# Kernel tuning notes

Hardware: AMD Instinct MI355X
Metric: run time of the kernel (lower is better)

The kernel has to match this reference:

```python
import jax, jax.numpy as jnp
import numpy as np

EPS = 1e-5

def conv2x2(x, w, b):
    # x: NCHW, w: OIHW (2x2), stride 2, valid padding
    y = jax.lax.conv_general_dilated(x, w, window_strides=(2, 2), padding='VALID',
                                     dimension_numbers=('NCHW', 'OIHW', 'NCHW'))
    return y + b[None, :, None, None]

def instancenorm(x):
    # per-sample, per-channel norm over H,W; biased variance, no affine (PyTorch defaults)
    mu = jnp.mean(x, axis=(2, 3), keepdims=True)
    var = jnp.mean(jnp.square(x - mu), axis=(2, 3), keepdims=True)
    return (x - mu) * jax.lax.rsqrt(var + EPS)

def lrelu(x):
    return jax.nn.leaky_relu(x, negative_slope=0.01)

def setup_inputs() -> dict:
    key = jax.random.key(0)
    ks = jax.random.split(key, 14)
    B, L = 256, 20
    s = 0.05
    inp = {
        'x': jax.random.normal(ks[0], (B, 3, 128, 128), jnp.float32),
        'labels': jax.random.uniform(ks[1], (B, L), jnp.float32),
        'w1': jax.random.normal(ks[2], (16, 3, 2, 2), jnp.float32) * s,
        'b1': jnp.zeros((16,), jnp.float32),
        'w2': jax.random.normal(ks[3], (32, 16 + L, 2, 2), jnp.float32) * s,
        'b2': jnp.zeros((32,), jnp.float32),
        'w3': jax.random.normal(ks[4], (64, 32, 2, 2), jnp.float32) * s,
        'b3': jnp.zeros((64,), jnp.float32),
        'w4': jax.random.normal(ks[5], (128, 64, 2, 2), jnp.float32) * s,
        'b4': jnp.zeros((128,), jnp.float32),
        'fcw1': jax.random.normal(ks[6], (1024, 128 * 8 * 8), jnp.float32) * s,
        'fcb1': jnp.zeros((1024,), jnp.float32),
        'fcw2': jax.random.normal(ks[7], (1, 1024), jnp.float32) * s,
        'fcb2': jnp.zeros((1,), jnp.float32),
    }
    return inp

def reference(x, labels, w1, b1, w2, b2, w3, b3, w4, b4, fcw1, fcb1, fcw2, fcb2):
    h = lrelu(instancenorm(conv2x2(x, w1, b1)))            # [B,16,64,64]
    # vectorized replacement of the per-element label broadcast loop
    lab = jnp.broadcast_to(labels[:, :, None, None],
                           (h.shape[0], labels.shape[1], h.shape[2], h.shape[3]))
    h = jnp.concatenate([h, lab], axis=1)                  # [B,36,64,64]
    h = lrelu(instancenorm(conv2x2(h, w2, b2)))            # [B,32,32,32]
    h = lrelu(instancenorm(conv2x2(h, w3, b3)))            # [B,64,16,16]
    h = lrelu(instancenorm(conv2x2(h, w4, b4)))            # [B,128,8,8]
    h = h.reshape(h.shape[0], -1)                          # [B,8192]
    h = lrelu(h @ fcw1.T + fcb1)                           # [B,1024]
    return h @ fcw2.T + fcb2                               # [B,1]
```

## Files before the change

kernel.cpp:

```cpp
#include <hip/hip_runtime.h>

#define EPSI 1e-5f

typedef __attribute__((ext_vector_type(8))) short bf16x8;
typedef __attribute__((ext_vector_type(4))) float f32x4;

__device__ __forceinline__ float lrelu(float x) { return x > 0.f ? x : 0.01f * x; }

__device__ __forceinline__ unsigned short f2bf(float x) {
    unsigned int u = __float_as_uint(x);
    return (unsigned short)((u + 0x7fffu + ((u >> 16) & 1u)) >> 16);
}
__device__ __forceinline__ float bflo(unsigned int v) { return __uint_as_float(v << 16); }
__device__ __forceinline__ float bfhi(unsigned int v) { return __uint_as_float(v & 0xFFFF0000u); }
__device__ __forceinline__ unsigned int pack2(float a, float b) {
    return (unsigned int)f2bf(a) | ((unsigned int)f2bf(b) << 16);
}
__device__ __forceinline__ bf16x8 pack8(float4 a, float4 b) {
    union { unsigned short u[8]; bf16x8 v; } p;
    p.u[0] = f2bf(a.x); p.u[1] = f2bf(a.y); p.u[2] = f2bf(a.z); p.u[3] = f2bf(a.w);
    p.u[4] = f2bf(b.x); p.u[5] = f2bf(b.y); p.u[6] = f2bf(b.z); p.u[7] = f2bf(b.w);
    return p.v;
}

__device__ __forceinline__ float2 block_reduce_sum2(float a, float b) {
    #pragma unroll
    for (int off = 1; off < 64; off <<= 1) {
        a += __shfl_xor(a, off, 64);
        b += __shfl_xor(b, off, 64);
    }
    __shared__ float lds[8];
    const int t = threadIdx.x;
    if ((t & 63) == 0) { lds[2 * (t >> 6)] = a; lds[2 * (t >> 6) + 1] = b; }
    __syncthreads();
    a = lds[0] + lds[2] + lds[4] + lds[6];
    b = lds[1] + lds[3] + lds[5] + lds[7];
    return make_float2(a, b);
}


__global__ __launch_bounds__(1024) void wprep(const float* __restrict__ w2,
                                              const float* __restrict__ w3,
                                              const float* __restrict__ w4,
                                              unsigned short* __restrict__ wk) {
    const int g = blockIdx.x * 1024 + threadIdx.x;
    if (g < 2048) {
        const int co = g >> 6, k = g & 63;
        const int ic = (k >> 4) * 4 + (k & 3), row = (k >> 3) & 1, tx = (k >> 2) & 1;
        wk[g] = f2bf(w2[co * 144 + ic * 4 + row * 2 + tx]);
    } else if (g < 10240) {
        const int e = g - 2048, co = e >> 7, k = e & 127;
        const int ic = (k >> 4) * 4 + (k & 3), row = (k >> 3) & 1, tx = (k >> 2) & 1;
        wk[g] = f2bf(w3[co * 128 + ic * 4 + row * 2 + tx]);
    } else if (g < 43008) {
        const int e = g - 10240, co = e >> 8, k = e & 255;
        const int ic = (k >> 4) * 4 + (k & 3), row = (k >> 3) & 1, tx = (k >> 2) & 1;
        wk[g] = f2bf(w4[co * 256 + ic * 4 + row * 2 + tx]);
    }
}

__global__ __launch_bounds__(1024, 1) void k1_conv_in(const float* __restrict__ x,
                                                      const float* __restrict__ w1,
                                                      unsigned short* __restrict__ h1) {
    const int n = blockIdx.x;
    const int t = threadIdx.x;
    __shared__ float red[16][16][2];
    __shared__ float msc[16][2];
    const float* xn = x + (size_t)n * 49152;
    float acc[16][4];
    #pragma unroll
    for (int j = 0; j < 16; ++j)
        #pragma unroll
        for (int q = 0; q < 4; ++q) acc[j][q] = 0.f;
    #pragma unroll 1
    for (int ic = 0; ic < 3; ++ic) {
        const float* p = xn + ic * 16384;
        float2 v0[4], v1[4];
        #pragma unroll
        for (int q = 0; q < 4; ++q) {
            const int idx = t + 1024 * q;
            const int oy = idx >> 6, ox = idx & 63;
            v0[q] = ((const float2*)(p + (2 * oy) * 128))[ox];
            v1[q] = ((const float2*)(p + (2 * oy + 1) * 128))[ox];
        }
        #pragma unroll
        for (int j = 0; j < 16; ++j) {
            const float4 wv = *(const float4*)(w1 + j * 12 + ic * 4);
            #pragma unroll
            for (int q = 0; q < 4; ++q)
                acc[j][q] += v0[q].x * wv.x + v0[q].y * wv.y + v1[q].x * wv.z + v1[q].y * wv.w;
        }
    }
    const int w = t >> 6, l = t & 63;
    #pragma unroll
    for (int j = 0; j < 16; ++j) {
        float s1 = acc[j][0] + acc[j][1] + acc[j][2] + acc[j][3];
        float s2 = acc[j][0] * acc[j][0] + acc[j][1] * acc[j][1] +
                   acc[j][2] * acc[j][2] + acc[j][3] * acc[j][3];
        #pragma unroll
        for (int off = 1; off < 64; off <<= 1) {
            s1 += __shfl_xor(s1, off, 64);
            s2 += __shfl_xor(s2, off, 64);
        }
        if (l == 0) { red[w][j][0] = s1; red[w][j][1] = s2; }
    }
    __syncthreads();
    if (t < 16) {
        float s1 = 0.f, s2 = 0.f;
        #pragma unroll
        for (int ww = 0; ww < 16; ++ww) { s1 += red[ww][t][0]; s2 += red[ww][t][1]; }
        const float mean = s1 * (1.f / 4096.f);
        const float var = s2 * (1.f / 4096.f) - mean * mean;
        msc[t][0] = mean; msc[t][1] = rsqrtf(var + EPSI);
    }
    __syncthreads();
    unsigned short* on = h1 + (size_t)n * 65536;
    #pragma unroll
    for (int q = 0; q < 4; ++q) {
        const int px = t + 1024 * q;
        #pragma unroll
        for (int q4 = 0; q4 < 4; ++q4) {
            const float n0 = lrelu((acc[4 * q4 + 0][q] - msc[4 * q4 + 0][0]) * msc[4 * q4 + 0][1]);
            const float n1 = lrelu((acc[4 * q4 + 1][q] - msc[4 * q4 + 1][0]) * msc[4 * q4 + 1][1]);
            const float n2 = lrelu((acc[4 * q4 + 2][q] - msc[4 * q4 + 2][0]) * msc[4 * q4 + 2][1]);
            const float n3 = lrelu((acc[4 * q4 + 3][q] - msc[4 * q4 + 3][0]) * msc[4 * q4 + 3][1]);
            uint2 u; u.x = pack2(n0, n1); u.y = pack2(n2, n3);
            *(uint2*)(on + ((size_t)q4 * 4096 + px) * 4) = u;
        }
    }
}

__global__ __launch_bounds__(1024, 1) void k2m(const unsigned short* __restrict__ h1,
                                               const unsigned short* __restrict__ wk,
                                               unsigned short* __restrict__ h2) {
    const int n = blockIdx.x;
    const int t = threadIdx.x;
    const int w = t >> 6, l = t & 63;
    __shared__ float red[16][32][2];
    __shared__ float msc[32][2];
    const unsigned short* h1n = h1 + (size_t)n * 65536;
    bf16x8 af[2][2];
    #pragma unroll
    for (int cf = 0; cf < 2; ++cf)
        #pragma unroll
        for (int ks = 0; ks < 2; ++ks)
            af[cf][ks] = *(const bf16x8*)(wk + (cf * 16 + (l & 15)) * 64 + ks * 32 + (l >> 4) * 8);
    f32x4 acc[4][2];
    const f32x4 z = {0.f, 0.f, 0.f, 0.f};
    #pragma unroll
    for (int pg = 0; pg < 4; ++pg) { acc[pg][0] = z; acc[pg][1] = z; }
    const int row = (l >> 4) & 1, icq0 = (l >> 4) >> 1;
    #pragma unroll
    for (int pg = 0; pg < 4; ++pg) {
        const int oy = 2 * w + (pg >> 1);
        const int ox = (pg & 1) * 16 + (l & 15);
        #pragma unroll
        for (int ks = 0; ks < 2; ++ks) {
            const bf16x8 bv = *(const bf16x8*)(h1n + (ks * 2 + icq0) * 16384 + (2 * oy + row) * 256 + ox * 8);
            acc[pg][0] = __builtin_amdgcn_mfma_f32_16x16x32_bf16(af[0][ks], bv, acc[pg][0], 0, 0, 0);
            acc[pg][1] = __builtin_amdgcn_mfma_f32_16x16x32_bf16(af[1][ks], bv, acc[pg][1], 0, 0, 0);
        }
    }
    #pragma unroll
    for (int cf = 0; cf < 2; ++cf) {
        #pragma unroll
        for (int r = 0; r < 4; ++r) {
            float s1 = acc[0][cf][r] + acc[1][cf][r] + acc[2][cf][r] + acc[3][cf][r];
            float s2 = acc[0][cf][r] * acc[0][cf][r] + acc[1][cf][r] * acc[1][cf][r] +
                       acc[2][cf][r] * acc[2][cf][r] + acc[3][cf][r] * acc[3][cf][r];
            #pragma unroll
            for (int off = 1; off < 16; off <<= 1) {
                s1 += __shfl_xor(s1, off, 64);
                s2 += __shfl_xor(s2, off, 64);
            }
            if ((l & 15) == 0) {
                red[w][cf * 16 + (l >> 4) * 4 + r][0] = s1;
                red[w][cf * 16 + (l >> 4) * 4 + r][1] = s2;
            }
        }
    }
    __syncthreads();
    if (t < 32) {
        float s1 = 0.f, s2 = 0.f;
        #pragma unroll
        for (int ww = 0; ww < 16; ++ww) { s1 += red[ww][t][0]; s2 += red[ww][t][1]; }
        const float mean = s1 * (1.f / 1024.f);
        const float var = s2 * (1.f / 1024.f) - mean * mean;
        msc[t][0] = mean; msc[t][1] = rsqrtf(var + EPSI);
    }
    __syncthreads();
    unsigned short* on = h2 + (size_t)n * 32768;
    #pragma unroll
    for (int pg = 0; pg < 4; ++pg) {
        const int px = w * 64 + pg * 16 + (l & 15);
        #pragma unroll
        for (int cf = 0; cf < 2; ++cf) {
            const int co0 = cf * 16 + (l >> 4) * 4;
            float v[4];
            #pragma unroll
            for (int r = 0; r < 4; ++r)
                v[r] = lrelu((acc[pg][cf][r] - msc[co0 + r][0]) * msc[co0 + r][1]);
            uint2 u; u.x = pack2(v[0], v[1]); u.y = pack2(v[2], v[3]);
            *(uint2*)(on + ((size_t)(cf * 4 + (l >> 4)) * 1024 + px) * 4) = u;
        }
    }
}

__global__ __launch_bounds__(1024, 1) void k3m(const unsigned short* __restrict__ h2,
                                               const unsigned short* __restrict__ wk,
                                               unsigned short* __restrict__ h3) {
    const int n = blockIdx.x;
    const int t = threadIdx.x;
    const int w = t >> 6, l = t & 63;
    __shared__ float red[16][64][2];
    __shared__ float msc[64][2];
    const unsigned short* h2n = h2 + (size_t)n * 32768;
    f32x4 acc[4];
    const f32x4 z = {0.f, 0.f, 0.f, 0.f};
    #pragma unroll
    for (int cf = 0; cf < 4; ++cf) acc[cf] = z;
    const int row = (l >> 4) & 1, icq0 = (l >> 4) >> 1;
    #pragma unroll
    for (int ks = 0; ks < 4; ++ks) {
        const bf16x8 bv = *(const bf16x8*)(h2n + (ks * 2 + icq0) * 4096 + (2 * w + row) * 128 + (l & 15) * 8);
        #pragma unroll
        for (int cf = 0; cf < 4; ++cf) {
            const bf16x8 af = *(const bf16x8*)(wk + (cf * 16 + (l & 15)) * 128 + ks * 32 + (l >> 4) * 8);
            acc[cf] = __builtin_amdgcn_mfma_f32_16x16x32_bf16(af, bv, acc[cf], 0, 0, 0);
        }
    }
    #pragma unroll
    for (int cf = 0; cf < 4; ++cf) {
        #pragma unroll
        for (int r = 0; r < 4; ++r) {
            float s1 = acc[cf][r], s2 = acc[cf][r] * acc[cf][r];
            #pragma unroll
            for (int off = 1; off < 16; off <<= 1) {
                s1 += __shfl_xor(s1, off, 64);
                s2 += __shfl_xor(s2, off, 64);
            }
            if ((l & 15) == 0) {
                red[w][cf * 16 + (l >> 4) * 4 + r][0] = s1;
                red[w][cf * 16 + (l >> 4) * 4 + r][1] = s2;
            }
        }
    }
    __syncthreads();
    if (t < 64) {
        float s1 = 0.f, s2 = 0.f;
        #pragma unroll
        for (int ww = 0; ww < 16; ++ww) { s1 += red[ww][t][0]; s2 += red[ww][t][1]; }
        const float mean = s1 * (1.f / 256.f);
        const float var = s2 * (1.f / 256.f) - mean * mean;
        msc[t][0] = mean; msc[t][1] = rsqrtf(var + EPSI);
    }
    __syncthreads();
    unsigned short* on = h3 + (size_t)n * 16384;
    const int px = w * 16 + (l & 15);
    #pragma unroll
    for (int cf = 0; cf < 4; ++cf) {
        const int co0 = cf * 16 + (l >> 4) * 4;
        float v[4];
        #pragma unroll
        for (int r = 0; r < 4; ++r)
            v[r] = lrelu((acc[cf][r] - msc[co0 + r][0]) * msc[co0 + r][1]);
        uint2 u; u.x = pack2(v[0], v[1]); u.y = pack2(v[2], v[3]);
        *(uint2*)(on + ((size_t)(cf * 4 + (l >> 4)) * 256 + px) * 4) = u;
    }
}

__global__ __launch_bounds__(512, 2) void k4m(const unsigned short* __restrict__ h3,
                                              const unsigned short* __restrict__ wk,
                                              unsigned short* __restrict__ h4) {
    const int n = blockIdx.x;
    const int t = threadIdx.x;
    const int w = t >> 6, l = t & 63;
    const int cfp = w & 3, khalf = w >> 2;
    __shared__ float ps[4][64][32];
    const unsigned short* h3n = h3 + (size_t)n * 16384;
    f32x4 acc[4][2];
    const f32x4 z = {0.f, 0.f, 0.f, 0.f};
    #pragma unroll
    for (int pg = 0; pg < 4; ++pg) { acc[pg][0] = z; acc[pg][1] = z; }
    const int row = (l >> 4) & 1, icq0 = (l >> 4) >> 1;
    const int oyb = (l & 15) >> 3, ox = l & 7;
    #pragma unroll
    for (int ksl = 0; ksl < 4; ++ksl) {
        const int ks = khalf * 4 + ksl;
        bf16x8 af0 = *(const bf16x8*)(wk + ((cfp * 2 + 0) * 16 + (l & 15)) * 256 + ks * 32 + (l >> 4) * 8);
        bf16x8 af1 = *(const bf16x8*)(wk + ((cfp * 2 + 1) * 16 + (l & 15)) * 256 + ks * 32 + (l >> 4) * 8);
        #pragma unroll
        for (int pg = 0; pg < 4; ++pg) {
            const int oy = pg * 2 + oyb;
            const bf16x8 bv = *(const bf16x8*)(h3n + (ks * 2 + icq0) * 1024 + (2 * oy + row) * 64 + ox * 8);
            acc[pg][0] = __builtin_amdgcn_mfma_f32_16x16x32_bf16(af0, bv, acc[pg][0], 0, 0, 0);
            acc[pg][1] = __builtin_amdgcn_mfma_f32_16x16x32_bf16(af1, bv, acc[pg][1], 0, 0, 0);
        }
    }
    if (khalf == 0) {
        #pragma unroll
        for (int pg = 0; pg < 4; ++pg)
            #pragma unroll
            for (int cfi = 0; cfi < 2; ++cfi)
                #pragma unroll
                for (int r = 0; r < 4; ++r)
                    ps[cfp][l][pg * 8 + cfi * 4 + r] = acc[pg][cfi][r];
    }
    __syncthreads();
    if (khalf == 1) {
        unsigned short* on = h4 + (size_t)n * 8192;
        #pragma unroll
        for (int cfi = 0; cfi < 2; ++cfi) {
            #pragma unroll
            for (int r = 0; r < 4; ++r) {
                float v[4];
                #pragma unroll
                for (int pg = 0; pg < 4; ++pg)
                    v[pg] = acc[pg][cfi][r] + ps[cfp][l][pg * 8 + cfi * 4 + r];
                float s1 = v[0] + v[1] + v[2] + v[3];
                float s2 = v[0] * v[0] + v[1] * v[1] + v[2] * v[2] + v[3] * v[3];
                #pragma unroll
                for (int off = 1; off < 16; off <<= 1) {
                    s1 += __shfl_xor(s1, off, 64);
                    s2 += __shfl_xor(s2, off, 64);
                }
                const float mean = s1 * (1.f / 64.f);
                const float var = s2 * (1.f / 64.f) - mean * mean;
                const float sc = rsqrtf(var + EPSI);
                const int co = (cfp * 2 + cfi) * 16 + (l >> 4) * 4 + r;
                #pragma unroll
                for (int pg = 0; pg < 4; ++pg)
                    on[co * 64 + pg * 16 + (l & 15)] = f2bf(lrelu((v[pg] - mean) * sc));
            }
        }
    }
}

__global__ __launch_bounds__(256, 2) void k5_fc1(const unsigned short* __restrict__ A,
                                                 const float* __restrict__ Wf,
                                                 float* __restrict__ Cp) {
    __shared__ unsigned short As[128 * 72];
    __shared__ unsigned short Bs[128 * 72];
    const int t = threadIdx.x;
    const int sk = blockIdx.x >> 4;
    const int tile = blockIdx.x & 15;
    const int mt = tile >> 3, nt = tile & 7;
    const int m0 = mt * 128, n0 = nt * 128;
    const int w = t >> 6, l = t & 63;
    const int wm = (w >> 1) * 64, wn = (w & 1) * 64;
    const int lr16 = l & 15, lk8 = (l >> 4) * 8;
    const int srow = t >> 3, scol = (t & 7) * 8;
    f32x4 acc[4][4];
    const f32x4 z = {0.f, 0.f, 0.f, 0.f};
    #pragma unroll
    for (int f = 0; f < 4; ++f)
        #pragma unroll
        for (int g = 0; g < 4; ++g) acc[f][g] = z;
    const int kbeg = sk * 512;
    #pragma unroll 1
    for (int kt = 0; kt < 8; ++kt) {
        const int kc = kbeg + kt * 64;
        bf16x8 av[4], bv[4];
        #pragma unroll
        for (int i = 0; i < 4; ++i) {
            av[i] = *(const bf16x8*)(A + (size_t)(m0 + srow + 32 * i) * 8192 + kc + scol);
            const float4 w0 = *(const float4*)(Wf + (size_t)(n0 + srow + 32 * i) * 8192 + kc + scol);
            const float4 w1 = *(const float4*)(Wf + (size_t)(n0 + srow + 32 * i) * 8192 + kc + scol + 4);
            bv[i] = pack8(w0, w1);
        }
        __syncthreads();
        #pragma unroll
        for (int i = 0; i < 4; ++i) {
            *(bf16x8*)&As[(srow + 32 * i) * 72 + scol] = av[i];
            *(bf16x8*)&Bs[(srow + 32 * i) * 72 + scol] = bv[i];
        }
        __syncthreads();
        #pragma unroll
        for (int ks = 0; ks < 2; ++ks) {
            bf16x8 af[4], bfr[4];
            #pragma unroll
            for (int f = 0; f < 4; ++f)
                af[f] = *(const bf16x8*)&As[(wm + f * 16 + lr16) * 72 + ks * 32 + lk8];
            #pragma unroll
            for (int g = 0; g < 4; ++g)
                bfr[g] = *(const bf16x8*)&Bs[(wn + g * 16 + lr16) * 72 + ks * 32 + lk8];
            #pragma unroll
            for (int f = 0; f < 4; ++f)
                #pragma unroll
                for (int g = 0; g < 4; ++g)
                    acc[f][g] = __builtin_amdgcn_mfma_f32_16x16x32_bf16(af[f], bfr[g], acc[f][g], 0, 0, 0);
        }
    }
    const int orow = (l >> 4) * 4, ocol = l & 15;
    #pragma unroll
    for (int f = 0; f < 4; ++f) {
        #pragma unroll
        for (int g = 0; g < 4; ++g) {
            #pragma unroll
            for (int j = 0; j < 4; ++j) {
                const int m = m0 + wm + f * 16 + orow + j;
                const int nn = n0 + wn + g * 16 + ocol;
                Cp[((size_t)sk * 256 + m) * 1024 + nn] = acc[f][g][j];
            }
        }
    }
}

__global__ __launch_bounds__(256) void k6_fc2(const float* __restrict__ Cp,
                                              const float* __restrict__ bias,
                                              const float* __restrict__ w,
                                              const float* __restrict__ b,
                                              float* __restrict__ out) {
    const int n = blockIdx.x, t = threadIdx.x;
    float part = 0.f;
    #pragma unroll
    for (int i = 0; i < 4; ++i) {
        const int nn = t + 256 * i;
        float s = 0.f;
        #pragma unroll
        for (int sk = 0; sk < 16; ++sk)
            s += Cp[((size_t)sk * 256 + n) * 1024 + nn];
        part += lrelu(s + bias[nn]) * w[nn];
    }
    const float2 red = block_reduce_sum2(part, 0.f);
    if (t == 0) out[n] = red.x + b[0];
}

extern "C" void kernel_launch(void* const* d_in, const int* in_sizes, int n_in,
                              void* d_out, int out_size, void* d_ws, size_t ws_size,
                              hipStream_t stream) {
    (void)in_sizes; (void)n_in; (void)out_size; (void)ws_size;
    const float* x    = (const float*)d_in[0];
    const float* w1   = (const float*)d_in[2];
    const float* w2   = (const float*)d_in[4];
    const float* w3   = (const float*)d_in[6];
    const float* w4   = (const float*)d_in[8];
    const float* fcw1 = (const float*)d_in[10];
    const float* fcb1 = (const float*)d_in[11];
    const float* fcw2 = (const float*)d_in[12];
    const float* fcb2 = (const float*)d_in[13];
    float* out = (float*)d_out;
    float* bufA = (float*)d_ws;
    float* bufB = bufA + 16777216;
    unsigned short* h1 = (unsigned short*)bufA;
    unsigned short* h2 = (unsigned short*)bufB;
    unsigned short* h3 = (unsigned short*)bufA;
    unsigned short* h4 = (unsigned short*)bufB;
    unsigned short* wk = (unsigned short*)bufB + 12582912;
    float* Cp = bufA;
    wprep<<<42, 1024, 0, stream>>>(w2, w3, w4, wk);
    k1_conv_in<<<256, 1024, 0, stream>>>(x, w1, h1);
    k2m<<<256, 1024, 0, stream>>>(h1, wk, h2);
    k3m<<<256, 1024, 0, stream>>>(h2, wk + 2048, h3);
    k4m<<<256, 512, 0, stream>>>(h3, wk + 10240, h4);
    k5_fc1<<<256, 256, 0, stream>>>(h4, fcw1, Cp);
    k6_fc2<<<256, 256, 0, stream>>>(Cp, fcb1, fcw2, fcb2, out);
}
```

Baseline: 92.56 us.

## Fuse conv layers 2-4 into one kernel keeping intermediates in LDS

```diff
diff --git a/kernel.cpp b/kernel.cpp
--- a/kernel.cpp
+++ b/kernel.cpp
@@ -11,8 +11,6 @@
     unsigned int u = __float_as_uint(x);
     return (unsigned short)((u + 0x7fffu + ((u >> 16) & 1u)) >> 16);
 }
-__device__ __forceinline__ float bflo(unsigned int v) { return __uint_as_float(v << 16); }
-__device__ __forceinline__ float bfhi(unsigned int v) { return __uint_as_float(v & 0xFFFF0000u); }
 __device__ __forceinline__ unsigned int pack2(float a, float b) {
     return (unsigned int)f2bf(a) | ((unsigned int)f2bf(b) << 16);
 }
@@ -130,207 +128,203 @@
     }
 }
 
-__global__ __launch_bounds__(1024, 1) void k2m(const unsigned short* __restrict__ h1,
-                                               const unsigned short* __restrict__ wk,
-                                               unsigned short* __restrict__ h2) {
+__global__ __launch_bounds__(1024, 1) void k234(const unsigned short* __restrict__ h1,
+                                                const unsigned short* __restrict__ wk,
+                                                unsigned short* __restrict__ h4) {
     const int n = blockIdx.x;
     const int t = threadIdx.x;
     const int w = t >> 6, l = t & 63;
-    __shared__ float red[16][32][2];
-    __shared__ float msc[32][2];
-    const unsigned short* h1n = h1 + (size_t)n * 65536;
-    bf16x8 af[2][2];
-    #pragma unroll
-    for (int cf = 0; cf < 2; ++cf)
-        #pragma unroll
-        for (int ks = 0; ks < 2; ++ks)
-            af[cf][ks] = *(const bf16x8*)(wk + (cf * 16 + (l & 15)) * 64 + ks * 32 + (l >> 4) * 8);
-    f32x4 acc[4][2];
-    const f32x4 z = {0.f, 0.f, 0.f, 0.f};
-    #pragma unroll
-    for (int pg = 0; pg < 4; ++pg) { acc[pg][0] = z; acc[pg][1] = z; }
-    const int row = (l >> 4) & 1, icq0 = (l >> 4) >> 1;
-    #pragma unroll
-    for (int pg = 0; pg < 4; ++pg) {
-        const int oy = 2 * w + (pg >> 1);
-        const int ox = (pg & 1) * 16 + (l & 15);
-        #pragma unroll
-        for (int ks = 0; ks < 2; ++ks) {
-            const bf16x8 bv = *(const bf16x8*)(h1n + (ks * 2 + icq0) * 16384 + (2 * oy + row) * 256 + ox * 8);
-            acc[pg][0] = __builtin_amdgcn_mfma_f32_16x16x32_bf16(af[0][ks], bv, acc[pg][0], 0, 0, 0);
-            acc[pg][1] = __builtin_amdgcn_mfma_f32_16x16x32_bf16(af[1][ks], bv, acc[pg][1], 0, 0, 0);
-        }
-    }
-    #pragma unroll
-    for (int cf = 0; cf < 2; ++cf) {
-        #pragma unroll
-        for (int r = 0; r < 4; ++r) {
-            float s1 = acc[0][cf][r] + acc[1][cf][r] + acc[2][cf][r] + acc[3][cf][r];
-            float s2 = acc[0][cf][r] * acc[0][cf][r] + acc[1][cf][r] * acc[1][cf][r] +
-                       acc[2][cf][r] * acc[2][cf][r] + acc[3][cf][r] * acc[3][cf][r];
-            #pragma unroll
-            for (int off = 1; off < 16; off <<= 1) {
-                s1 += __shfl_xor(s1, off, 64);
-                s2 += __shfl_xor(s2, off, 64);
-            }
-            if ((l & 15) == 0) {
-                red[w][cf * 16 + (l >> 4) * 4 + r][0] = s1;
-                red[w][cf * 16 + (l >> 4) * 4 + r][1] = s2;
-            }
-        }
-    }
-    __syncthreads();
-    if (t < 32) {
-        float s1 = 0.f, s2 = 0.f;
-        #pragma unroll
-        for (int ww = 0; ww < 16; ++ww) { s1 += red[ww][t][0]; s2 += red[ww][t][1]; }
-        const float mean = s1 * (1.f / 1024.f);
-        const float var = s2 * (1.f / 1024.f) - mean * mean;
-        msc[t][0] = mean; msc[t][1] = rsqrtf(var + EPSI);
-    }
-    __syncthreads();
-    unsigned short* on = h2 + (size_t)n * 32768;
-    #pragma unroll
-    for (int pg = 0; pg < 4; ++pg) {
-        const int px = w * 64 + pg * 16 + (l & 15);
-        #pragma unroll
-        for (int cf = 0; cf < 2; ++cf) {
-            const int co0 = cf * 16 + (l >> 4) * 4;
-            float v[4];
-            #pragma unroll
-            for (int r = 0; r < 4; ++r)
-                v[r] = lrelu((acc[pg][cf][r] - msc[co0 + r][0]) * msc[co0 + r][1]);
-            uint2 u; u.x = pack2(v[0], v[1]); u.y = pack2(v[2], v[3]);
-            *(uint2*)(on + ((size_t)(cf * 4 + (l >> 4)) * 1024 + px) * 4) = u;
-        }
-    }
-}
-
-__global__ __launch_bounds__(1024, 1) void k3m(const unsigned short* __restrict__ h2,
-                                               const unsigned short* __restrict__ wk,
-                                               unsigned short* __restrict__ h3) {
-    const int n = blockIdx.x;
-    const int t = threadIdx.x;
-    const int w = t >> 6, l = t & 63;
+    __shared__ unsigned short h2s[32768];
+    __shared__ unsigned short h3s[16384];
+    __shared__ float ps[4][64][32];
     __shared__ float red[16][64][2];
     __shared__ float msc[64][2];
-    const unsigned short* h2n = h2 + (size_t)n * 32768;
-    f32x4 acc[4];
-    const f32x4 z = {0.f, 0.f, 0.f, 0.f};
-    #pragma unroll
-    for (int cf = 0; cf < 4; ++cf) acc[cf] = z;
-    const int row = (l >> 4) & 1, icq0 = (l >> 4) >> 1;
-    #pragma unroll
-    for (int ks = 0; ks < 4; ++ks) {
-        const bf16x8 bv = *(const bf16x8*)(h2n + (ks * 2 + icq0) * 4096 + (2 * w + row) * 128 + (l & 15) * 8);
-        #pragma unroll
-        for (int cf = 0; cf < 4; ++cf) {
-            const bf16x8 af = *(const bf16x8*)(wk + (cf * 16 + (l & 15)) * 128 + ks * 32 + (l >> 4) * 8);
-            acc[cf] = __builtin_amdgcn_mfma_f32_16x16x32_bf16(af, bv, acc[cf], 0, 0, 0);
-        }
-    }
-    #pragma unroll
-    for (int cf = 0; cf < 4; ++cf) {
-        #pragma unroll
-        for (int r = 0; r < 4; ++r) {
-            float s1 = acc[cf][r], s2 = acc[cf][r] * acc[cf][r];
-            #pragma unroll
-            for (int off = 1; off < 16; off <<= 1) {
-                s1 += __shfl_xor(s1, off, 64);
-                s2 += __shfl_xor(s2, off, 64);
-            }
-            if ((l & 15) == 0) {
-                red[w][cf * 16 + (l >> 4) * 4 + r][0] = s1;
-                red[w][cf * 16 + (l >> 4) * 4 + r][1] = s2;
-            }
-        }
-    }
-    __syncthreads();
-    if (t < 64) {
-        float s1 = 0.f, s2 = 0.f;
-        #pragma unroll
-        for (int ww = 0; ww < 16; ++ww) { s1 += red[ww][t][0]; s2 += red[ww][t][1]; }
-        const float mean = s1 * (1.f / 256.f);
-        const float var = s2 * (1.f / 256.f) - mean * mean;
-        msc[t][0] = mean; msc[t][1] = rsqrtf(var + EPSI);
-    }
-    __syncthreads();
-    unsigned short* on = h3 + (size_t)n * 16384;
-    const int px = w * 16 + (l & 15);
-    #pragma unroll
-    for (int cf = 0; cf < 4; ++cf) {
-        const int co0 = cf * 16 + (l >> 4) * 4;
-        float v[4];
-        #pragma unroll
-        for (int r = 0; r < 4; ++r)
-            v[r] = lrelu((acc[cf][r] - msc[co0 + r][0]) * msc[co0 + r][1]);
-        uint2 u; u.x = pack2(v[0], v[1]); u.y = pack2(v[2], v[3]);
-        *(uint2*)(on + ((size_t)(cf * 4 + (l >> 4)) * 256 + px) * 4) = u;
-    }
-}
-
-__global__ __launch_bounds__(512, 2) void k4m(const unsigned short* __restrict__ h3,
-                                              const unsigned short* __restrict__ wk,
-                                              unsigned short* __restrict__ h4) {
-    const int n = blockIdx.x;
-    const int t = threadIdx.x;
-    const int w = t >> 6, l = t & 63;
-    const int cfp = w & 3, khalf = w >> 2;
-    __shared__ float ps[4][64][32];
-    const unsigned short* h3n = h3 + (size_t)n * 16384;
-    f32x4 acc[4][2];
-    const f32x4 z = {0.f, 0.f, 0.f, 0.f};
-    #pragma unroll
-    for (int pg = 0; pg < 4; ++pg) { acc[pg][0] = z; acc[pg][1] = z; }
-    const int row = (l >> 4) & 1, icq0 = (l >> 4) >> 1;
-    const int oyb = (l & 15) >> 3, ox = l & 7;
-    #pragma unroll
-    for (int ksl = 0; ksl < 4; ++ksl) {
-        const int ks = khalf * 4 + ksl;
-        bf16x8 af0 = *(const bf16x8*)(wk + ((cfp * 2 + 0) * 16 + (l & 15)) * 256 + ks * 32 + (l >> 4) * 8);
-        bf16x8 af1 = *(const bf16x8*)(wk + ((cfp * 2 + 1) * 16 + (l & 15)) * 256 + ks * 32 + (l >> 4) * 8);
+    const unsigned short* h1n = h1 + (size_t)n * 65536;
+
+    {
+        const unsigned short* wk2 = wk;
+        bf16x8 af[2][2];
+        #pragma unroll
+        for (int cf = 0; cf < 2; ++cf)
+            #pragma unroll
+            for (int ks = 0; ks < 2; ++ks)
+                af[cf][ks] = *(const bf16x8*)(wk2 + (cf * 16 + (l & 15)) * 64 + ks * 32 + (l >> 4) * 8);
+        f32x4 acc[4][2];
+        const f32x4 z = {0.f, 0.f, 0.f, 0.f};
+        #pragma unroll
+        for (int pg = 0; pg < 4; ++pg) { acc[pg][0] = z; acc[pg][1] = z; }
+        const int row = (l >> 4) & 1, icq0 = (l >> 4) >> 1;
         #pragma unroll
         for (int pg = 0; pg < 4; ++pg) {
-            const int oy = pg * 2 + oyb;
-            const bf16x8 bv = *(const bf16x8*)(h3n + (ks * 2 + icq0) * 1024 + (2 * oy + row) * 64 + ox * 8);
-            acc[pg][0] = __builtin_amdgcn_mfma_f32_16x16x32_bf16(af0, bv, acc[pg][0], 0, 0, 0);
-            acc[pg][1] = __builtin_amdgcn_mfma_f32_16x16x32_bf16(af1, bv, acc[pg][1], 0, 0, 0);
-        }
-    }
-    if (khalf == 0) {
-        #pragma unroll
-        for (int pg = 0; pg < 4; ++pg)
-            #pragma unroll
-            for (int cfi = 0; cfi < 2; ++cfi)
-                #pragma unroll
-                for (int r = 0; r < 4; ++r)
-                    ps[cfp][l][pg * 8 + cfi * 4 + r] = acc[pg][cfi][r];
-    }
-    __syncthreads();
-    if (khalf == 1) {
-        unsigned short* on = h4 + (size_t)n * 8192;
-        #pragma unroll
-        for (int cfi = 0; cfi < 2; ++cfi) {
+            const int oy = 2 * w + (pg >> 1);
+            const int ox = (pg & 1) * 16 + (l & 15);
+            #pragma unroll
+            for (int ks = 0; ks < 2; ++ks) {
+                const bf16x8 bv = *(const bf16x8*)(h1n + (ks * 2 + icq0) * 16384 + (2 * oy + row) * 256 + ox * 8);
+                acc[pg][0] = __builtin_amdgcn_mfma_f32_16x16x32_bf16(af[0][ks], bv, acc[pg][0], 0, 0, 0);
+                acc[pg][1] = __builtin_amdgcn_mfma_f32_16x16x32_bf16(af[1][ks], bv, acc[pg][1], 0, 0, 0);
+            }
+        }
+        #pragma unroll
+        for (int cf = 0; cf < 2; ++cf) {
             #pragma unroll
             for (int r = 0; r < 4; ++r) {
-                float v[4];
-                #pragma unroll
-                for (int pg = 0; pg < 4; ++pg)
-                    v[pg] = acc[pg][cfi][r] + ps[cfp][l][pg * 8 + cfi * 4 + r];
-                float s1 = v[0] + v[1] + v[2] + v[3];
-                float s2 = v[0] * v[0] + v[1] * v[1] + v[2] * v[2] + v[3] * v[3];
+                float s1 = acc[0][cf][r] + acc[1][cf][r] + acc[2][cf][r] + acc[3][cf][r];
+                float s2 = acc[0][cf][r] * acc[0][cf][r] + acc[1][cf][r] * acc[1][cf][r] +
+                           acc[2][cf][r] * acc[2][cf][r] + acc[3][cf][r] * acc[3][cf][r];
                 #pragma unroll
                 for (int off = 1; off < 16; off <<= 1) {
                     s1 += __shfl_xor(s1, off, 64);
                     s2 += __shfl_xor(s2, off, 64);
                 }
-                const float mean = s1 * (1.f / 64.f);
-                const float var = s2 * (1.f / 64.f) - mean * mean;
-                const float sc = rsqrtf(var + EPSI);
-                const int co = (cfp * 2 + cfi) * 16 + (l >> 4) * 4 + r;
-                #pragma unroll
-                for (int pg = 0; pg < 4; ++pg)
-                    on[co * 64 + pg * 16 + (l & 15)] = f2bf(lrelu((v[pg] - mean) * sc));
+                if ((l & 15) == 0) {
+                    red[w][cf * 16 + (l >> 4) * 4 + r][0] = s1;
+                    red[w][cf * 16 + (l >> 4) * 4 + r][1] = s2;
+                }
+            }
+        }
+        __syncthreads();
+        if (t < 32) {
+            float s1 = 0.f, s2 = 0.f;
+            #pragma unroll
+            for (int ww = 0; ww < 16; ++ww) { s1 += red[ww][t][0]; s2 += red[ww][t][1]; }
+            const float mean = s1 * (1.f / 1024.f);
+            const float var = s2 * (1.f / 1024.f) - mean * mean;
+            msc[t][0] = mean; msc[t][1] = rsqrtf(var + EPSI);
+        }
+        __syncthreads();
+        #pragma unroll
+        for (int pg = 0; pg < 4; ++pg) {
+            const int px = w * 64 + pg * 16 + (l & 15);
+            #pragma unroll
+            for (int cf = 0; cf < 2; ++cf) {
+                const int co0 = cf * 16 + (l >> 4) * 4;
+                float v[4];
+                #pragma unroll
+                for (int r = 0; r < 4; ++r)
+                    v[r] = lrelu((acc[pg][cf][r] - msc[co0 + r][0]) * msc[co0 + r][1]);
+                uint2 u; u.x = pack2(v[0], v[1]); u.y = pack2(v[2], v[3]);
+                *(uint2*)(&h2s[((cf * 4 + (l >> 4)) * 1024 + px) * 4]) = u;
+            }
+        }
+    }
+    __syncthreads();
+
+    {
+        const unsigned short* wk3 = wk + 2048;
+        f32x4 acc[4];
+        const f32x4 z = {0.f, 0.f, 0.f, 0.f};
+        #pragma unroll
+        for (int cf = 0; cf < 4; ++cf) acc[cf] = z;
+        const int row = (l >> 4) & 1, icq0 = (l >> 4) >> 1;
+        #pragma unroll
+        for (int ks = 0; ks < 4; ++ks) {
+            const bf16x8 bv = *(const bf16x8*)(&h2s[(ks * 2 + icq0) * 4096 + (2 * w + row) * 128 + (l & 15) * 8]);
+            #pragma unroll
+            for (int cf = 0; cf < 4; ++cf) {
+                const bf16x8 af = *(const bf16x8*)(wk3 + (cf * 16 + (l & 15)) * 128 + ks * 32 + (l >> 4) * 8);
+                acc[cf] = __builtin_amdgcn_mfma_f32_16x16x32_bf16(af, bv, acc[cf], 0, 0, 0);
+            }
+        }
+        #pragma unroll
+        for (int cf = 0; cf < 4; ++cf) {
+            #pragma unroll
+            for (int r = 0; r < 4; ++r) {
+                float s1 = acc[cf][r], s2 = acc[cf][r] * acc[cf][r];
+                #pragma unroll
+                for (int off = 1; off < 16; off <<= 1) {
+                    s1 += __shfl_xor(s1, off, 64);
+                    s2 += __shfl_xor(s2, off, 64);
+                }
+                if ((l & 15) == 0) {
+                    red[w][cf * 16 + (l >> 4) * 4 + r][0] = s1;
+                    red[w][cf * 16 + (l >> 4) * 4 + r][1] = s2;
+                }
+            }
+        }
+        __syncthreads();
+        if (t < 64) {
+            float s1 = 0.f, s2 = 0.f;
+            #pragma unroll
+            for (int ww = 0; ww < 16; ++ww) { s1 += red[ww][t][0]; s2 += red[ww][t][1]; }
+            const float mean = s1 * (1.f / 256.f);
+            const float var = s2 * (1.f / 256.f) - mean * mean;
+            msc[t][0] = mean; msc[t][1] = rsqrtf(var + EPSI);
+        }
+        __syncthreads();
+        const int px = w * 16 + (l & 15);
+        #pragma unroll
+        for (int cf = 0; cf < 4; ++cf) {
+            const int co0 = cf * 16 + (l >> 4) * 4;
+            float v[4];
+            #pragma unroll
+            for (int r = 0; r < 4; ++r)
+                v[r] = lrelu((acc[cf][r] - msc[co0 + r][0]) * msc[co0 + r][1]);
+            uint2 u; u.x = pack2(v[0], v[1]); u.y = pack2(v[2], v[3]);
+            *(uint2*)(&h3s[((cf * 4 + (l >> 4)) * 256 + px) * 4]) = u;
+        }
+    }
+    __syncthreads();
+
+    {
+        const unsigned short* wk4 = wk + 10240;
+        const int cfp = w & 3, khalf = (w >> 2) & 1;
+        f32x4 acc[4][2];
+        const f32x4 z = {0.f, 0.f, 0.f, 0.f};
+        #pragma unroll
+        for (int pg = 0; pg < 4; ++pg) { acc[pg][0] = z; acc[pg][1] = z; }
+        const int row = (l >> 4) & 1, icq0 = (l >> 4) >> 1;
+        const int oyb = (l & 15) >> 3, ox = l & 7;
+        if (w < 8) {
+            #pragma unroll
+            for (int ksl = 0; ksl < 4; ++ksl) {
+                const int ks = khalf * 4 + ksl;
+                bf16x8 af0 = *(const bf16x8*)(wk4 + ((cfp * 2 + 0) * 16 + (l & 15)) * 256 + ks * 32 + (l >> 4) * 8);
+                bf16x8 af1 = *(const bf16x8*)(wk4 + ((cfp * 2 + 1) * 16 + (l & 15)) * 256 + ks * 32 + (l >> 4) * 8);
+                #pragma unroll
+                for (int pg = 0; pg < 4; ++pg) {
+                    const int oy = pg * 2 + oyb;
+                    const bf16x8 bv = *(const bf16x8*)(&h3s[(ks * 2 + icq0) * 1024 + (2 * oy + row) * 64 + ox * 8]);
+                    acc[pg][0] = __builtin_amdgcn_mfma_f32_16x16x32_bf16(af0, bv, acc[pg][0], 0, 0, 0);
+                    acc[pg][1] = __builtin_amdgcn_mfma_f32_16x16x32_bf16(af1, bv, acc[pg][1], 0, 0, 0);
+                }
+            }
+        }
+        if (w < 4) {
+            #pragma unroll
+            for (int pg = 0; pg < 4; ++pg)
+                #pragma unroll
+                for (int cfi = 0; cfi < 2; ++cfi)
+                    #pragma unroll
+                    for (int r = 0; r < 4; ++r)
+                        ps[cfp][l][pg * 8 + cfi * 4 + r] = acc[pg][cfi][r];
+        }
+        __syncthreads();
+        if (w >= 4 && w < 8) {
+            unsigned short* on = h4 + (size_t)n * 8192;
+            #pragma unroll
+            for (int cfi = 0; cfi < 2; ++cfi) {
+                #pragma unroll
+                for (int r = 0; r < 4; ++r) {
+                    float v[4];
+                    #pragma unroll
+                    for (int pg = 0; pg < 4; ++pg)
+                        v[pg] = acc[pg][cfi][r] + ps[cfp][l][pg * 8 + cfi * 4 + r];
+                    float s1 = v[0] + v[1] + v[2] + v[3];
+                    float s2 = v[0] * v[0] + v[1] * v[1] + v[2] * v[2] + v[3] * v[3];
+                    #pragma unroll
+                    for (int off = 1; off < 16; off <<= 1) {
+                        s1 += __shfl_xor(s1, off, 64);
+                        s2 += __shfl_xor(s2, off, 64);
+                    }
+                    const float mean = s1 * (1.f / 64.f);
+                    const float var = s2 * (1.f / 64.f) - mean * mean;
+                    const float sc = rsqrtf(var + EPSI);
+                    const int co = (cfp * 2 + cfi) * 16 + (l >> 4) * 4 + r;
+                    #pragma unroll
+                    for (int pg = 0; pg < 4; ++pg)
+                        on[co * 64 + pg * 16 + (l & 15)] = f2bf(lrelu((v[pg] - mean) * sc));
+                }
             }
         }
     }
@@ -443,16 +437,12 @@
     float* bufA = (float*)d_ws;
     float* bufB = bufA + 16777216;
     unsigned short* h1 = (unsigned short*)bufA;
-    unsigned short* h2 = (unsigned short*)bufB;
-    unsigned short* h3 = (unsigned short*)bufA;
     unsigned short* h4 = (unsigned short*)bufB;
     unsigned short* wk = (unsigned short*)bufB + 12582912;
     float* Cp = bufA;
     wprep<<<42, 1024, 0, stream>>>(w2, w3, w4, wk);
     k1_conv_in<<<256, 1024, 0, stream>>>(x, w1, h1);
-    k2m<<<256, 1024, 0, stream>>>(h1, wk, h2);
-    k3m<<<256, 1024, 0, stream>>>(h2, wk + 2048, h3);
-    k4m<<<256, 512, 0, stream>>>(h3, wk + 10240, h4);
+    k234<<<256, 1024, 0, stream>>>(h1, wk, h4);
     k5_fc1<<<256, 256, 0, stream>>>(h4, fcw1, Cp);
     k6_fc2<<<256, 256, 0, stream>>>(Cp, fcb1, fcw2, fcb2, out);
 }
```

New measurement: 83.86 us. -9.4%, faster.
